# Optimization experiments

Measured on AMD Instinct MI355X. Metric: run time of the kernel, lower is better.

## Reference

```python
import jax, jax.numpy as jnp
import numpy as np

LN_EPS = 1e-5

def _layer_norm(x, g, b):
    mu = jnp.mean(x, axis=-1, keepdims=True)
    var = jnp.var(x, axis=-1, keepdims=True)
    return (x - mu) * jax.lax.rsqrt(var + LN_EPS) * g + b

def _mlp(x, W1, b1, g1, beta1, W2, b2):
    h = x @ W1 + b1
    h = _layer_norm(h, g1, beta1)
    h = jax.nn.silu(h)
    return h @ W2 + b2

def setup_inputs() -> dict:
    key = jax.random.key(0)
    ks = jax.random.split(key, 16)
    N, E = 50000, 600000
    node_dim, edge_dim, hidden = 128, 128, 256
    def lin(k, fan_in, fan_out):
        bound = 1.0 / np.sqrt(fan_in)
        kw, kb = jax.random.split(k)
        W = jax.random.uniform(kw, (fan_in, fan_out), jnp.float32, -bound, bound)
        b = jax.random.uniform(kb, (fan_out,), jnp.float32, -bound, bound)
        return W, b
    eW1, eb1 = lin(ks[0], 2 * node_dim + edge_dim, hidden)
    eW2, eb2 = lin(ks[1], hidden, edge_dim)
    nW1, nb1 = lin(ks[2], node_dim + edge_dim, hidden)
    nW2, nb2 = lin(ks[3], hidden, node_dim)
    return {
        "node_features": jax.random.normal(ks[4], (N, node_dim), jnp.float32),
        "edge_features": jax.random.normal(ks[5], (E, edge_dim), jnp.float32),
        "edge_index": jax.random.randint(ks[6], (2, E), 0, N, jnp.int64),
        "eW1": eW1, "eb1": eb1, "eg1": jnp.ones((hidden,), jnp.float32), "ebeta1": jnp.zeros((hidden,), jnp.float32),
        "eW2": eW2, "eb2": eb2,
        "nW1": nW1, "nb1": nb1, "ng1": jnp.ones((hidden,), jnp.float32), "nbeta1": jnp.zeros((hidden,), jnp.float32),
        "nW2": nW2, "nb2": nb2,
    }

def reference(node_features, edge_features, edge_index,
              eW1, eb1, eg1, ebeta1, eW2, eb2,
              nW1, nb1, ng1, nbeta1, nW2, nb2):
    senders = edge_index[0]
    receivers = edge_index[1]
    # gather -> edge MLP (residual)
    edge_input = jnp.concatenate(
        [node_features[senders], node_features[receivers], edge_features], axis=-1)  # [E, 2*nd+ed]
    edge_features = edge_features + _mlp(edge_input, eW1, eb1, eg1, ebeta1, eW2, eb2)
    # scatter-add aggregate over receivers
    n_nodes = node_features.shape[0]
    aggregated = jax.ops.segment_sum(edge_features, receivers, num_segments=n_nodes)
    # node MLP (residual)
    node_input = jnp.concatenate([node_features, aggregated], axis=-1)  # [N, nd+ed]
    node_features = node_features + _mlp(node_input, nW1, nb1, ng1, nbeta1, nW2, nb2)
    return node_features, edge_features
```

## Files before the change

kernel.cpp:

```cpp
#include <hip/hip_runtime.h>

#define N_NODES 50000
#define N_EDGES 600000
#define DIM 128
#define HID 256
#define MR 32

typedef float  f32x4  __attribute__((ext_vector_type(4), aligned(16), may_alias));
typedef float  f32x2  __attribute__((ext_vector_type(2), aligned(8),  may_alias));
typedef __bf16 bf16x8 __attribute__((ext_vector_type(8), aligned(16), may_alias));
typedef int    i32x4  __attribute__((ext_vector_type(4), aligned(16), may_alias));

static __device__ inline f32x4 mfma16x16x32(bf16x8 a, bf16x8 b, f32x4 c) {
    return __builtin_amdgcn_mfma_f32_16x16x32_bf16(a, b, c, 0, 0, 0);
}

static __device__ inline bf16x8 cvt2_bf16(f32x4 a, f32x4 b) {
    bf16x8 o;
    o[0] = (__bf16)a[0]; o[1] = (__bf16)a[1]; o[2] = (__bf16)a[2]; o[3] = (__bf16)a[3];
    o[4] = (__bf16)b[0]; o[5] = (__bf16)b[1]; o[6] = (__bf16)b[2]; o[7] = (__bf16)b[3];
    return o;
}

static __device__ inline void pack_one(const float* __restrict__ W,
                                       __bf16* __restrict__ out,
                                       int idx, int Ncols) {
    int lane = idx & 63;
    int tc = idx >> 6;
    int nC = Ncols >> 4;
    int c = tc % nC;
    int t = tc / nC;
    int col = (c << 4) + (lane & 15);
    int k0 = (t << 5) + ((lane >> 4) << 3);
    bf16x8 v;
#pragma unroll
    for (int j = 0; j < 8; ++j) v[j] = (__bf16)W[(k0 + j) * Ncols + col];
    *((bf16x8*)out + idx) = v;
}

__global__ void prep_kernel(const float* __restrict__ node, __bf16* __restrict__ nbf,
                            const float* __restrict__ eW1, const float* __restrict__ eW2,
                            const float* __restrict__ nW1, const float* __restrict__ nW2,
                            __bf16* __restrict__ peW1, __bf16* __restrict__ peW2,
                            __bf16* __restrict__ pnW1, __bf16* __restrict__ pnW2,
                            const int* __restrict__ eidx, int* __restrict__ counts) {
    int b = blockIdx.x;
    if (b < 3125) {
        int idx = b * 256 + threadIdx.x;
        if (idx >= N_NODES * 16) return;
        int row = idx >> 4, c = idx & 15;
        const float* p = node + (size_t)row * DIM + (c << 3);
        f32x4 a = ((const f32x4*)p)[0], bb = ((const f32x4*)p)[1];
        *(bf16x8*)(nbf + (size_t)row * DIM + (c << 3)) = cvt2_bf16(a, bb);
    } else if (b < 3237) {
        int idx = (b - 3125) * 256 + threadIdx.x;
        if (idx < 12288)       pack_one(eW1, peW1, idx, 256);
        else if (idx < 16384)  pack_one(eW2, peW2, idx - 12288, 128);
        else if (idx < 24576)  pack_one(nW1, pnW1, idx - 16384, 256);
        else                   pack_one(nW2, pnW2, idx - 24576, 128);
    } else {
        int e = (b - 3237) * 256 + threadIdx.x;
        if (e < N_EDGES) {
            int r = eidx[N_EDGES + e];
            r = (r < 0) ? 0 : (r >= N_NODES ? N_NODES - 1 : r);
            atomicAdd(&counts[r], 1);
        }
    }
}

__global__ __launch_bounds__(1024) void scan_kernel(const int* __restrict__ counts,
                                                    int* __restrict__ offsets,
                                                    int* __restrict__ cursor) {
    __shared__ int part[1024];
    const int t = threadIdx.x;
    const int CH = (N_NODES + 1023) / 1024;
    const int base = t * CH;
    int s = 0;
#pragma unroll 1
    for (int i = 0; i < CH; ++i) {
        int idx = base + i;
        if (idx < N_NODES) s += counts[idx];
    }
    part[t] = s;
    __syncthreads();
    for (int d = 1; d < 1024; d <<= 1) {
        int x = (t >= d) ? part[t - d] : 0;
        __syncthreads();
        part[t] += x;
        __syncthreads();
    }
    int run = part[t] - s;
#pragma unroll 1
    for (int i = 0; i < CH; ++i) {
        int idx = base + i;
        if (idx < N_NODES) {
            offsets[idx] = run;
            cursor[idx]  = run;
            run += counts[idx];
        }
    }
    if (t == 1023) offsets[N_NODES] = run;
}

__global__ void scatter_kernel(const int* __restrict__ eidx,
                               int* __restrict__ cursor, int* __restrict__ eids) {
    int e = blockIdx.x * 256 + threadIdx.x;
    if (e < N_EDGES) {
        int r = eidx[N_EDGES + e];
        r = (r < 0) ? 0 : (r >= N_NODES ? N_NODES - 1 : r);
        int pos = atomicAdd(&cursor[r], 1);
        eids[pos] = e;
    }
}

template<int ASTRIDE, int T1>
__device__ inline void mlp_core(char* lds,
                                const bf16x8* __restrict__ pW1,
                                const bf16x8* __restrict__ pW2,
                                const float* __restrict__ b1,
                                const float* __restrict__ g1,
                                const float* __restrict__ be1,
                                f32x4 (&acc2)[2][2]) {
    const int tid = threadIdx.x;
    const int w = tid >> 6;
    const int lane = tid & 63;
    const int l16 = lane & 15;
    const int g = lane >> 4;
    float* stats = (float*)(lds + 32 * ASTRIDE);

    f32x4 acc[2][4];
#pragma unroll
    for (int m = 0; m < 2; ++m)
#pragma unroll
        for (int n = 0; n < 4; ++n) acc[m][n] = (f32x4){0.f, 0.f, 0.f, 0.f};
#pragma unroll
    for (int t = 0; t < T1; ++t) {
        bf16x8 af[2];
#pragma unroll
        for (int m = 0; m < 2; ++m)
            af[m] = *(const bf16x8*)(lds + (m * 16 + l16) * ASTRIDE + t * 64 + g * 16);
        const bf16x8* bp = pW1 + ((t * 16 + 4 * w) << 6) + lane;
#pragma unroll
        for (int n = 0; n < 4; ++n) {
            bf16x8 bf = bp[n << 6];
#pragma unroll
            for (int m = 0; m < 2; ++m)
                acc[m][n] = mfma16x16x32(af[m], bf, acc[m][n]);
        }
    }

    float b1v[4];
#pragma unroll
    for (int n = 0; n < 4; ++n) b1v[n] = b1[64 * w + 16 * n + l16];
#pragma unroll
    for (int m = 0; m < 2; ++m) {
#pragma unroll
        for (int n = 0; n < 4; ++n) acc[m][n] += b1v[n];
        f32x4 s = (acc[m][0] + acc[m][1]) + (acc[m][2] + acc[m][3]);
        f32x4 q = acc[m][0] * acc[m][0];
        q = acc[m][1] * acc[m][1] + q;
        q = acc[m][2] * acc[m][2] + q;
        q = acc[m][3] * acc[m][3] + q;
#pragma unroll
        for (int st = 1; st <= 8; st <<= 1) {
#pragma unroll
            for (int r = 0; r < 4; ++r) {
                s[r] += __shfl_xor(s[r], st);
                q[r] += __shfl_xor(q[r], st);
            }
        }
        if (l16 == 0) {
#pragma unroll
            for (int r = 0; r < 4; ++r) {
                int row = m * 16 + g * 4 + r;
                *(f32x2*)(stats + row * 8 + w * 2) = (f32x2){s[r], q[r]};
            }
        }
    }
    __syncthreads();

    f32x4 mu4[2], rs4[2];
#pragma unroll
    for (int m = 0; m < 2; ++m)
#pragma unroll
        for (int r = 0; r < 4; ++r) {
            int row = m * 16 + g * 4 + r;
            f32x4 a = *(const f32x4*)(stats + row * 8);
            f32x4 b = *(const f32x4*)(stats + row * 8 + 4);
            float S = (a[0] + a[2]) + (b[0] + b[2]);
            float Q = (a[1] + a[3]) + (b[1] + b[3]);
            float mm = S * (1.f / 256.f);
            float vv = fmaxf(Q * (1.f / 256.f) - mm * mm, 0.f);
            mu4[m][r] = mm;
            rs4[m][r] = __builtin_amdgcn_rsqf(vv + 1e-5f);
        }
    float g1v[4], bev[4];
#pragma unroll
    for (int n = 0; n < 4; ++n) {
        g1v[n] = g1[64 * w + 16 * n + l16];
        bev[n] = be1[64 * w + 16 * n + l16];
    }
#pragma unroll
    for (int m = 0; m < 2; ++m)
#pragma unroll
        for (int n = 0; n < 4; ++n) {
            f32x4 y = (acc[m][n] - mu4[m]) * rs4[m];
            y = y * g1v[n] + bev[n];
            int col = 64 * w + 16 * n + l16;
#pragma unroll
            for (int r = 0; r < 4; ++r) {
                float e = __builtin_amdgcn_exp2f(y[r] * -1.44269504f);
                float x = y[r] * __builtin_amdgcn_rcpf(1.f + e);
                int row = m * 16 + g * 4 + r;
                *(__bf16*)(lds + row * 528 + col * 2) = (__bf16)x;
            }
        }
    __syncthreads();

#pragma unroll
    for (int m = 0; m < 2; ++m)
#pragma unroll
        for (int n = 0; n < 2; ++n) acc2[m][n] = (f32x4){0.f, 0.f, 0.f, 0.f};
#pragma unroll
    for (int t = 0; t < 8; ++t) {
        bf16x8 af[2];
#pragma unroll
        for (int m = 0; m < 2; ++m)
            af[m] = *(const bf16x8*)(lds + (m * 16 + l16) * 528 + t * 64 + g * 16);
        const bf16x8* bp = pW2 + ((t * 8 + 2 * w) << 6) + lane;
#pragma unroll
        for (int n = 0; n < 2; ++n) {
            bf16x8 bf = bp[n << 6];
#pragma unroll
            for (int m = 0; m < 2; ++m)
                acc2[m][n] = mfma16x16x32(af[m], bf, acc2[m][n]);
        }
    }
}

__global__ __launch_bounds__(256, 5) void edge_kernel(
    const __bf16* __restrict__ nbf, const float* __restrict__ ef,
    const int* __restrict__ eidx,
    const bf16x8* __restrict__ pW1, const bf16x8* __restrict__ pW2,
    const float* __restrict__ b1, const float* __restrict__ g1,
    const float* __restrict__ be1, const float* __restrict__ b2,
    float* __restrict__ out_edges) {
    __shared__ __align__(16) char lds[MR * 784 + MR * 32];
    const int tid = threadIdx.x;
    const int eb = blockIdx.x * MR;

    {
        int row = tid >> 3, l8 = tid & 7;
        int e = eb + row;
        int snd = eidx[e], rcv = eidx[N_EDGES + e];
        snd = (snd < 0) ? 0 : (snd >= N_NODES ? N_NODES - 1 : snd);
        rcv = (rcv < 0) ? 0 : (rcv >= N_NODES ? N_NODES - 1 : rcv);
        const char* ps = (const char*)(nbf + (size_t)snd * DIM) + (l8 << 5);
        const char* pr = (const char*)(nbf + (size_t)rcv * DIM) + (l8 << 5);
        char* dst = lds + row * 784 + (l8 << 5);
        *(i32x4*)dst         = *(const i32x4*)ps;
        *(i32x4*)(dst + 16)  = *(const i32x4*)(ps + 16);
        *(i32x4*)(dst + 256) = *(const i32x4*)pr;
        *(i32x4*)(dst + 272) = *(const i32x4*)(pr + 16);
        const float* pe = ef + (size_t)e * DIM + (l8 << 4);
        f32x4 a0 = ((const f32x4*)pe)[0], a1 = ((const f32x4*)pe)[1];
        f32x4 a2 = ((const f32x4*)pe)[2], a3 = ((const f32x4*)pe)[3];
        *(bf16x8*)(dst + 512) = cvt2_bf16(a0, a1);
        *(bf16x8*)(dst + 528) = cvt2_bf16(a2, a3);
    }
    __syncthreads();

    f32x4 acc2[2][2];
    mlp_core<784, 12>(lds, pW1, pW2, b1, g1, be1, acc2);

    {
        const int w = tid >> 6, lane = tid & 63;
        const int l16 = lane & 15, g = lane >> 4;
        float b2v[2];
#pragma unroll
        for (int n = 0; n < 2; ++n) b2v[n] = b2[32 * w + 16 * n + l16];
#pragma unroll
        for (int m = 0; m < 2; ++m)
#pragma unroll
            for (int n = 0; n < 2; ++n)
#pragma unroll
                for (int r = 0; r < 4; ++r) {
                    int e = eb + m * 16 + g * 4 + r;
                    int col = 32 * w + 16 * n + l16;
                    size_t off = (size_t)e * DIM + col;
                    out_edges[off] = acc2[m][n][r] + b2v[n] + ef[off];
                }
    }
}

__global__ __launch_bounds__(256, 8) void node_kernel(
    const float* __restrict__ node, const __bf16* __restrict__ nbf,
    const float* __restrict__ out_edges,
    const int* __restrict__ offsets, const int* __restrict__ eids,
    const bf16x8* __restrict__ pW1, const bf16x8* __restrict__ pW2,
    const float* __restrict__ b1, const float* __restrict__ g1,
    const float* __restrict__ be1, const float* __restrict__ b2,
    float* __restrict__ out_nodes) {
    __shared__ __align__(16) char lds[MR * 528 + MR * 32];
    const int tid = threadIdx.x;
    const int nb = blockIdx.x * MR;

    {
        int row = tid >> 3, l8 = tid & 7;
        int n = nb + row;
        int nc = (n > N_NODES - 1) ? N_NODES - 1 : n;
        const char* pn = (const char*)(nbf + (size_t)nc * DIM) + (l8 << 5);
        char* dst = lds + row * 528 + (l8 << 5);
        *(i32x4*)dst        = *(const i32x4*)pn;
        *(i32x4*)(dst + 16) = *(const i32x4*)(pn + 16);
        float a[16];
#pragma unroll
        for (int j = 0; j < 16; ++j) a[j] = 0.f;
        int st = offsets[nc], en = offsets[nc + 1];
        int i = st;
#pragma unroll 1
        for (; i + 2 <= en; i += 2) {
            int e0 = eids[i], e1 = eids[i + 1];
            const float* er0 = out_edges + (size_t)e0 * DIM + (l8 << 4);
            const float* er1 = out_edges + (size_t)e1 * DIM + (l8 << 4);
            f32x4 u0 = ((const f32x4*)er0)[0], u1 = ((const f32x4*)er0)[1];
            f32x4 u2 = ((const f32x4*)er0)[2], u3 = ((const f32x4*)er0)[3];
            f32x4 v0 = ((const f32x4*)er1)[0], v1 = ((const f32x4*)er1)[1];
            f32x4 v2 = ((const f32x4*)er1)[2], v3 = ((const f32x4*)er1)[3];
#pragma unroll
            for (int k = 0; k < 4; ++k) {
                a[0 + k]  += u0[k] + v0[k];
                a[4 + k]  += u1[k] + v1[k];
                a[8 + k]  += u2[k] + v2[k];
                a[12 + k] += u3[k] + v3[k];
            }
        }
        if (i < en) {
            int e0 = eids[i];
            const float* er0 = out_edges + (size_t)e0 * DIM + (l8 << 4);
#pragma unroll
            for (int k = 0; k < 4; ++k) {
                f32x4 v = ((const f32x4*)er0)[k];
                a[k * 4 + 0] += v[0]; a[k * 4 + 1] += v[1];
                a[k * 4 + 2] += v[2]; a[k * 4 + 3] += v[3];
            }
        }
        bf16x8 o0, o1;
#pragma unroll
        for (int j = 0; j < 8; ++j) { o0[j] = (__bf16)a[j]; o1[j] = (__bf16)a[8 + j]; }
        int cbase = 16 + (l8 << 1);
        *(bf16x8*)(lds + row * 528 + (cbase << 4)) = o0;
        *(bf16x8*)(lds + row * 528 + ((cbase + 1) << 4)) = o1;
    }
    __syncthreads();

    f32x4 acc2[2][2];
    mlp_core<528, 8>(lds, pW1, pW2, b1, g1, be1, acc2);

    {
        const int w = tid >> 6, lane = tid & 63;
        const int l16 = lane & 15, g = lane >> 4;
        float b2v[2];
#pragma unroll
        for (int n = 0; n < 2; ++n) b2v[n] = b2[32 * w + 16 * n + l16];
#pragma unroll
        for (int m = 0; m < 2; ++m)
#pragma unroll
            for (int n = 0; n < 2; ++n)
#pragma unroll
                for (int r = 0; r < 4; ++r) {
                    int nd = nb + m * 16 + g * 4 + r;
                    if (nd < N_NODES) {
                        int col = 32 * w + 16 * n + l16;
                        size_t off = (size_t)nd * DIM + col;
                        out_nodes[off] = acc2[m][n][r] + b2v[n] + node[off];
                    }
                }
    }
}

extern "C" void kernel_launch(void* const* d_in, const int* in_sizes, int n_in,
                              void* d_out, int out_size, void* d_ws, size_t ws_size,
                              hipStream_t stream) {
    const float* node  = (const float*)d_in[0];
    const float* ef    = (const float*)d_in[1];
    const int*   eidx  = (const int*)d_in[2];
    const float* eW1   = (const float*)d_in[3];
    const float* eb1   = (const float*)d_in[4];
    const float* eg1   = (const float*)d_in[5];
    const float* ebt1  = (const float*)d_in[6];
    const float* eW2   = (const float*)d_in[7];
    const float* eb2   = (const float*)d_in[8];
    const float* nW1   = (const float*)d_in[9];
    const float* nb1   = (const float*)d_in[10];
    const float* ng1   = (const float*)d_in[11];
    const float* nbt1  = (const float*)d_in[12];
    const float* nW2   = (const float*)d_in[13];
    const float* nb2   = (const float*)d_in[14];

    char* ws = (char*)d_ws;
    int* counts  = (int*)ws;
    int* offsets = counts + 50016;
    int* cursor  = offsets + 50016;
    int* eids    = cursor + 50016;
    char* nbase = (char*)(eids + 600064);
    __bf16* nbf = (__bf16*)(((uintptr_t)nbase + 255) & ~(uintptr_t)255);
    __bf16* peW1 = nbf + (size_t)N_NODES * DIM;
    __bf16* peW2 = peW1 + 384 * 256;
    __bf16* pnW1 = peW2 + 256 * 128;
    __bf16* pnW2 = pnW1 + 256 * 256;

    hipMemsetAsync(counts, 0, 50000 * sizeof(int), stream);
    prep_kernel<<<3125 + 112 + 2344, 256, 0, stream>>>(
        node, nbf, eW1, eW2, nW1, nW2, peW1, peW2, pnW1, pnW2, eidx, counts);
    scan_kernel<<<1, 1024, 0, stream>>>(counts, offsets, cursor);
    scatter_kernel<<<(N_EDGES + 255) / 256, 256, 0, stream>>>(eidx, cursor, eids);

    float* out_nodes = (float*)d_out;
    float* out_edges = out_nodes + (size_t)N_NODES * DIM;

    edge_kernel<<<N_EDGES / MR, 256, 0, stream>>>(
        nbf, ef, eidx, (const bf16x8*)peW1, (const bf16x8*)peW2,
        eb1, eg1, ebt1, eb2, out_edges);
    node_kernel<<<(N_NODES + MR - 1) / MR, 256, 0, stream>>>(
        node, nbf, out_edges, offsets, eids, (const bf16x8*)pnW1, (const bf16x8*)pnW2,
        nb1, ng1, nbt1, nb2, out_nodes);
}
```

Baseline: 631.2 us.

## Split neighbor aggregation into a separate wave-per-node kernel

Moves the CSR segment-sum of edge outputs out of the node MLP kernel into a dedicated agg_kernel. There one wavefront handles one node, and its four 16-lane groups stride over the edges, then combine partial sums with lane shuffles. The node kernel now just loads the precomputed fp32 aggregate and converts it to bf16, and its launch-bounds occupancy hint is lowered. The aim is more memory-level parallelism for the irregular gather, instead of 8 threads per node looping serially inside the MLP block. The cost is an extra kernel launch and a write and re-read of a 50000x128 fp32 buffer in the workspace.

```diff
diff --git a/kernel.cpp b/kernel.cpp
--- a/kernel.cpp
+++ b/kernel.cpp
@@ -113,6 +113,41 @@
     }
 }
 
+__global__ __launch_bounds__(256) void agg_kernel(
+    const float* __restrict__ out_edges,
+    const int* __restrict__ offsets, const int* __restrict__ eids,
+    float* __restrict__ agg) {
+    const int tid = threadIdx.x;
+    const int n = blockIdx.x * 4 + (tid >> 6);
+    const int lane = tid & 63;
+    const int es = lane >> 4;
+    const int cg = lane & 15;
+    float a[8];
+#pragma unroll
+    for (int j = 0; j < 8; ++j) a[j] = 0.f;
+    int st = offsets[n], en = offsets[n + 1];
+#pragma unroll 1
+    for (int i = st + es; i < en; i += 4) {
+        int e = eids[i];
+        const float* p = out_edges + (size_t)e * DIM + (cg << 3);
+        f32x4 v0 = ((const f32x4*)p)[0], v1 = ((const f32x4*)p)[1];
+        a[0] += v0[0]; a[1] += v0[1]; a[2] += v0[2]; a[3] += v0[3];
+        a[4] += v1[0]; a[5] += v1[1]; a[6] += v1[2]; a[7] += v1[3];
+    }
+#pragma unroll
+    for (int j = 0; j < 8; ++j) {
+        a[j] += __shfl_xor(a[j], 16);
+        a[j] += __shfl_xor(a[j], 32);
+    }
+    if (es == 0) {
+        float* q = agg + (size_t)n * DIM + (cg << 3);
+        f32x4 w0 = {a[0], a[1], a[2], a[3]};
+        f32x4 w1 = {a[4], a[5], a[6], a[7]};
+        ((f32x4*)q)[0] = w0;
+        ((f32x4*)q)[1] = w1;
+    }
+}
+
 template<int ASTRIDE, int T1>
 __device__ inline void mlp_core(char* lds,
                                 const bf16x8* __restrict__ pW1,
@@ -293,10 +328,9 @@
     }
 }
 
-__global__ __launch_bounds__(256, 8) void node_kernel(
+__global__ __launch_bounds__(256, 5) void node_kernel(
     const float* __restrict__ node, const __bf16* __restrict__ nbf,
-    const float* __restrict__ out_edges,
-    const int* __restrict__ offsets, const int* __restrict__ eids,
+    const float* __restrict__ agg,
     const bf16x8* __restrict__ pW1, const bf16x8* __restrict__ pW2,
     const float* __restrict__ b1, const float* __restrict__ g1,
     const float* __restrict__ be1, const float* __restrict__ b2,
@@ -313,44 +347,12 @@
         char* dst = lds + row * 528 + (l8 << 5);
         *(i32x4*)dst        = *(const i32x4*)pn;
         *(i32x4*)(dst + 16) = *(const i32x4*)(pn + 16);
-        float a[16];
-#pragma unroll
-        for (int j = 0; j < 16; ++j) a[j] = 0.f;
-        int st = offsets[nc], en = offsets[nc + 1];
-        int i = st;
-#pragma unroll 1
-        for (; i + 2 <= en; i += 2) {
-            int e0 = eids[i], e1 = eids[i + 1];
-            const float* er0 = out_edges + (size_t)e0 * DIM + (l8 << 4);
-            const float* er1 = out_edges + (size_t)e1 * DIM + (l8 << 4);
-            f32x4 u0 = ((const f32x4*)er0)[0], u1 = ((const f32x4*)er0)[1];
-            f32x4 u2 = ((const f32x4*)er0)[2], u3 = ((const f32x4*)er0)[3];
-            f32x4 v0 = ((const f32x4*)er1)[0], v1 = ((const f32x4*)er1)[1];
-            f32x4 v2 = ((const f32x4*)er1)[2], v3 = ((const f32x4*)er1)[3];
-#pragma unroll
-            for (int k = 0; k < 4; ++k) {
-                a[0 + k]  += u0[k] + v0[k];
-                a[4 + k]  += u1[k] + v1[k];
-                a[8 + k]  += u2[k] + v2[k];
-                a[12 + k] += u3[k] + v3[k];
-            }
-        }
-        if (i < en) {
-            int e0 = eids[i];
-            const float* er0 = out_edges + (size_t)e0 * DIM + (l8 << 4);
-#pragma unroll
-            for (int k = 0; k < 4; ++k) {
-                f32x4 v = ((const f32x4*)er0)[k];
-                a[k * 4 + 0] += v[0]; a[k * 4 + 1] += v[1];
-                a[k * 4 + 2] += v[2]; a[k * 4 + 3] += v[3];
-            }
-        }
-        bf16x8 o0, o1;
-#pragma unroll
-        for (int j = 0; j < 8; ++j) { o0[j] = (__bf16)a[j]; o1[j] = (__bf16)a[8 + j]; }
+        const float* ap = agg + (size_t)nc * DIM + (l8 << 4);
+        f32x4 a0 = ((const f32x4*)ap)[0], a1 = ((const f32x4*)ap)[1];
+        f32x4 a2 = ((const f32x4*)ap)[2], a3 = ((const f32x4*)ap)[3];
         int cbase = 16 + (l8 << 1);
-        *(bf16x8*)(lds + row * 528 + (cbase << 4)) = o0;
-        *(bf16x8*)(lds + row * 528 + ((cbase + 1) << 4)) = o1;
+        *(bf16x8*)(lds + row * 528 + (cbase << 4)) = cvt2_bf16(a0, a1);
+        *(bf16x8*)(lds + row * 528 + ((cbase + 1) << 4)) = cvt2_bf16(a2, a3);
     }
     __syncthreads();
 
@@ -403,8 +405,9 @@
     int* offsets = counts + 50016;
     int* cursor  = offsets + 50016;
     int* eids    = cursor + 50016;
-    char* nbase = (char*)(eids + 600064);
-    __bf16* nbf = (__bf16*)(((uintptr_t)nbase + 255) & ~(uintptr_t)255);
+    char* abase = (char*)(eids + 600064);
+    float* agg = (float*)(((uintptr_t)abase + 255) & ~(uintptr_t)255);
+    __bf16* nbf = (__bf16*)(agg + (size_t)N_NODES * DIM);
     __bf16* peW1 = nbf + (size_t)N_NODES * DIM;
     __bf16* peW2 = peW1 + 384 * 256;
     __bf16* pnW1 = peW2 + 256 * 128;
@@ -422,7 +425,8 @@
     edge_kernel<<<N_EDGES / MR, 256, 0, stream>>>(
         nbf, ef, eidx, (const bf16x8*)peW1, (const bf16x8*)peW2,
         eb1, eg1, ebt1, eb2, out_edges);
+    agg_kernel<<<N_NODES / 4, 256, 0, stream>>>(out_edges, offsets, eids, agg);
     node_kernel<<<(N_NODES + MR - 1) / MR, 256, 0, stream>>>(
-        node, nbf, out_edges, offsets, eids, (const bf16x8*)pnW1, (const bf16x8*)pnW2,
+        node, nbf, agg, (const bf16x8*)pnW1, (const bf16x8*)pnW2,
         nb1, ng1, nbt1, nb2, out_nodes);
 }
```

New measurement: 622.9 us. No clear change (-1.3%).
